# Kernel tuning notes

Hardware: AMD Instinct MI355X
Metric: run time of the kernel (lower is better)

## Reference

```python
import jax, jax.numpy as jnp
import numpy as np

N_NODES = 50000


def _glorot(key, fan_in, fan_out):
    limit = float(np.sqrt(6.0 / (fan_in + fan_out)))
    return jax.random.uniform(key, (fan_in, fan_out), jnp.float32, -limit, limit)


def setup_inputs() -> dict:
    key = jax.random.key(0)
    k_x, k_src, k_dst, k1, k2, k3 = jax.random.split(key, 6)
    x = jax.random.normal(k_x, (N_NODES, 128), dtype=jnp.float32)
    src = jax.random.randint(k_src, (800000,), 0, N_NODES)
    dst = jax.random.randint(k_dst, (800000,), 0, N_NODES)
    edge_index = jnp.stack([src, dst]).astype(jnp.int64)  # [2, E]
    W1 = _glorot(k1, 128, 96)
    W2 = _glorot(k2, 96, 96)
    W3 = _glorot(k3, 96, 40)
    b1 = jnp.zeros((96,), jnp.float32)
    b2 = jnp.zeros((96,), jnp.float32)
    b3 = jnp.zeros((40,), jnp.float32)
    return {"x": x, "W1": W1, "b1": b1, "W2": W2, "b2": b2,
            "W3": W3, "b3": b3, "edge_index": edge_index}


def _aggregate(x, src, dst):
    # sparse adj SpMM with 'add' reduce: out[dst] += x[src]
    return jax.ops.segment_sum(x[src], dst, num_segments=N_NODES)


def reference(x, W1, b1, W2, b2, W3, b3, edge_index):
    src, dst = edge_index[0], edge_index[1]
    # layer 1: aggregate -> linear -> relu (dropout identity in eval)
    h = jax.nn.relu(_aggregate(x, src, dst) @ W1 + b1)
    # layer 2
    h = jax.nn.relu(_aggregate(h, src, dst) @ W2 + b2)
    # layer 3 + log_softmax
    logits = _aggregate(h, src, dst) @ W3 + b3
    return jax.nn.log_softmax(logits, axis=-1)
```

## Files before the change

### kernel.cpp

```cpp
#include <hip/hip_runtime.h>
#include <math.h>

typedef __attribute__((ext_vector_type(8))) short bf16x8;
typedef __attribute__((ext_vector_type(4))) float f32x4;

__device__ __forceinline__ unsigned short f2bf(float f) {
  unsigned u = __float_as_uint(f);
  u += 0x7fffu + ((u >> 16) & 1u);
  return (unsigned short)(u >> 16);
}
__device__ __forceinline__ float bflo(unsigned u) { return __uint_as_float(u << 16); }
__device__ __forceinline__ float bfhi(unsigned u) { return __uint_as_float(u & 0xffff0000u); }


constexpr int CB = 64;

__global__ __launch_bounds__(256) void count_pack(const int* __restrict__ dst,
                                                  int* __restrict__ partial, int E,
                                                  const float* __restrict__ W1,
                                                  const float* __restrict__ W2,
                                                  const float* __restrict__ W3,
                                                  unsigned short* __restrict__ Wp1,
                                                  unsigned short* __restrict__ Wp2,
                                                  unsigned short* __restrict__ Wp3) {
  int tid = threadIdx.x;
  if (blockIdx.x < CB) {
    __shared__ int bkt[256];
    bkt[tid] = 0;
    __syncthreads();
    int E4 = E >> 2;
    const int4* d4 = (const int4*)dst;
    for (int i = blockIdx.x * 256 + tid; i < E4; i += CB * 256) {
      int4 d = d4[i];
      atomicAdd(&bkt[d.x >> 8], 1);
      atomicAdd(&bkt[d.y >> 8], 1);
      atomicAdd(&bkt[d.z >> 8], 1);
      atomicAdd(&bkt[d.w >> 8], 1);
    }
    if (blockIdx.x == 0 && tid < (E & 3)) atomicAdd(&bkt[dst[E4 * 4 + tid] >> 8], 1);
    __syncthreads();
    partial[blockIdx.x * 256 + tid] = bkt[tid];
    return;
  }
  int gid = (blockIdx.x - CB) * 256 + tid;
  const float* W;
  unsigned short* Wp;
  int t, NCTT, M, MV;
  if (gid < 1536) {
    W = W1; Wp = Wp1; t = gid; NCTT = 6; M = 96; MV = 96;
  } else if (gid < 2688) {
    W = W2; Wp = Wp2; t = gid - 1536; NCTT = 6; M = 96; MV = 96;
  } else if (gid < 3264) {
    W = W3; Wp = Wp3; t = gid - 2688; NCTT = 3; M = 40; MV = 40;
  } else {
    return;
  }
  int lane = t & 63;
  int frag = t >> 6;
  int s = frag / NCTT;
  int ct = frag - s * NCTT;
  int colv = ct * 16 + (lane & 15);
  int k0 = s * 32 + (lane >> 4) * 8;
  union { unsigned short s[8]; uint4 u; } pk;
#pragma unroll
  for (int j = 0; j < 8; ++j) {
    float v = (colv < MV) ? W[(k0 + j) * M + colv] : 0.f;
    pk.s[j] = f2bf(v);
  }
  ((uint4*)Wp)[t] = pk.u;
}

__global__ __launch_bounds__(256) void scan_kernel(const int* __restrict__ partial,
                                                   int* __restrict__ gstart,
                                                   int* __restrict__ gcur,
                                                   int* __restrict__ row_ptr,
                                                   int NB, int N, int E) {
  int tid = threadIdx.x;
  int s = 0;
#pragma unroll 8
  for (int i = 0; i < CB; ++i) s += partial[i * 256 + tid];
  __shared__ int sm[256];
  sm[tid] = s;
  __syncthreads();
  for (int off = 1; off < 256; off <<= 1) {
    int u = (tid >= off) ? sm[tid - off] : 0;
    __syncthreads();
    sm[tid] += u;
    __syncthreads();
  }
  int excl = sm[tid] - s;
  if (tid < NB) { gstart[tid] = excl; gcur[tid] = excl; }
  if (tid == NB - 1) gstart[NB] = sm[tid];
  if (tid == 0) row_ptr[N] = E;
}

__global__ __launch_bounds__(256) void bin_gemm1(const int* __restrict__ src,
                                                 const int* __restrict__ dst,
                                                 int* __restrict__ gcur,
                                                 int* __restrict__ packed, int E, int NB,
                                                 int NBIN, const float* __restrict__ x,
                                                 const unsigned short* __restrict__ Wp1,
                                                 unsigned short* __restrict__ Tb, int N) {
  int tid = threadIdx.x;
  if (blockIdx.x < NBIN) {
    __shared__ int lcnt[256];
    __shared__ int gbase[256];
    lcnt[tid] = 0;
    __syncthreads();
    int idx = blockIdx.x * 256 + tid;
    int E4 = E >> 2;
    int sv[4], dv[4], lv[4];
    int cnt = 0;
    if (idx < E4) {
      int4 s4 = ((const int4*)src)[idx];
      int4 d4 = ((const int4*)dst)[idx];
      sv[0] = s4.x; sv[1] = s4.y; sv[2] = s4.z; sv[3] = s4.w;
      dv[0] = d4.x; dv[1] = d4.y; dv[2] = d4.z; dv[3] = d4.w;
      cnt = 4;
    } else if (idx == E4 && (E & 3)) {
      int tl = E & 3;
      for (int i = 0; i < tl; ++i) { sv[i] = src[E4 * 4 + i]; dv[i] = dst[E4 * 4 + i]; }
      cnt = tl;
    }
    for (int i = 0; i < cnt; ++i) lv[i] = atomicAdd(&lcnt[dv[i] >> 8], 1);
    __syncthreads();
    if (tid < NB) gbase[tid] = atomicAdd(&gcur[tid], lcnt[tid]);
    __syncthreads();
    for (int i = 0; i < cnt; ++i) {
      int b = dv[i] >> 8;
      packed[gbase[b] + lv[i]] = ((dv[i] & 255) << 16) | (sv[i] & 0xffff);
    }
    return;
  }
  int bx = blockIdx.x - NBIN;
  int wid = tid >> 6;
  int lane = tid & 63;
  int rt = bx * 4 + wid;
  if (rt * 16 >= N) return;
  int quad = lane >> 4;
  int lm = lane & 15;
  union BU { uint4 u; bf16x8 v; };
  f32x4 acc[6];
#pragma unroll
  for (int c = 0; c < 6; ++c) acc[c] = (f32x4){0.f, 0.f, 0.f, 0.f};
  int row = rt * 16 + lm;
  if (row >= N) row = N - 1;
  const uint4* wp4 = (const uint4*)Wp1;
#pragma unroll
  for (int s = 0; s < 4; ++s) {
    int k0 = s * 32 + quad * 8;
    const float* Af = x + (size_t)row * 128 + k0;
    float4 x0 = *(const float4*)(Af);
    float4 x1 = *(const float4*)(Af + 4);
    union { unsigned short s[8]; bf16x8 v; } au;
    au.s[0] = f2bf(x0.x); au.s[1] = f2bf(x0.y); au.s[2] = f2bf(x0.z); au.s[3] = f2bf(x0.w);
    au.s[4] = f2bf(x1.x); au.s[5] = f2bf(x1.y); au.s[6] = f2bf(x1.z); au.s[7] = f2bf(x1.w);
#pragma unroll
    for (int c = 0; c < 6; ++c) {
      BU bu;
      bu.u = wp4[(s * 6 + c) * 64 + lane];
      acc[c] = __builtin_amdgcn_mfma_f32_16x16x32_bf16(au.v, bu.v, acc[c], 0, 0, 0);
    }
  }
#pragma unroll
  for (int c = 0; c < 6; ++c) {
    int colv = c * 16 + lm;
#pragma unroll
    for (int r = 0; r < 4; ++r) {
      int orow = rt * 16 + quad * 4 + r;
      if (orow < N) Tb[(size_t)orow * 96 + colv] = f2bf(acc[c][r]);
    }
  }
}

__global__ __launch_bounds__(256) void build_local_csr(const int* __restrict__ packed,
                                                       const int* __restrict__ gstart,
                                                       int* __restrict__ row_ptr,
                                                       int* __restrict__ col, int N) {
  __shared__ int cnt[256];
  __shared__ int sm[256];
  int b = blockIdx.x, tid = threadIdx.x;
  int gs = gstart[b], ge = gstart[b + 1];
  int me = ge - gs;
  int node0 = b << 8;
  int RL = N - node0;
  if (RL > 256) RL = 256;
  cnt[tid] = 0;
  __syncthreads();
  for (int i = tid; i < me; i += 256) atomicAdd(&cnt[packed[gs + i] >> 16], 1);
  __syncthreads();
  int v = cnt[tid];
  sm[tid] = v;
  __syncthreads();
  for (int off = 1; off < 256; off <<= 1) {
    int u = (tid >= off) ? sm[tid - off] : 0;
    __syncthreads();
    sm[tid] += u;
    __syncthreads();
  }
  int excl = gs + sm[tid] - v;
  __syncthreads();
  cnt[tid] = excl;
  if (tid < RL) row_ptr[node0 + tid] = excl;
  __syncthreads();
  for (int i = tid; i < me; i += 256) {
    int pk = packed[gs + i];
    int p = atomicAdd(&cnt[pk >> 16], 1);
    col[p] = pk & 0xffff;
  }
}


template <int NCT, int MOUT, int MVALID>
__global__ __launch_bounds__(256, 6) void fused_agg_gemm(
    const unsigned short* __restrict__ tin, const int* __restrict__ row_ptr,
    const int* __restrict__ col, const float* __restrict__ bias,
    const unsigned short* __restrict__ Wp, unsigned short* __restrict__ outp, int N) {
  constexpr int LST = 104;
  constexpr int CAP = 2048;
  __shared__ unsigned short sH[64 * LST];
  __shared__ int scol[CAP];
  __shared__ int srp[65];
  int tid = threadIdx.x;
  int node0 = blockIdx.x * 64;
  int nloc = N - node0;
  if (nloc > 64) nloc = 64;
  if (tid <= nloc) srp[tid] = row_ptr[node0 + tid];
  __syncthreads();
  int gs = srp[0];
  int me = srp[nloc] - gs;
  for (int i = tid; i < me && i < CAP; i += 256) scol[i] = col[gs + i];
  __syncthreads();

#pragma unroll
  for (int it = 0; it < 3; ++it) {
    int u = tid + it * 256;
    int nl = u / 12;
    int c = u - nl * 12;
    if (nl < nloc) {
      int beg = srp[nl] - gs;
      int end = srp[nl + 1] - gs;
      const unsigned short* tc = tin + 8 * c;
      float a0 = 0.f, a1 = 0.f, a2 = 0.f, a3 = 0.f, a4 = 0.f, a5 = 0.f, a6 = 0.f, a7 = 0.f;
      int e = beg;
      for (; e + 3 < end; e += 4) {
        int s0 = (e < CAP) ? scol[e] : col[gs + e];
        int s1 = (e + 1 < CAP) ? scol[e + 1] : col[gs + e + 1];
        int s2 = (e + 2 < CAP) ? scol[e + 2] : col[gs + e + 2];
        int s3 = (e + 3 < CAP) ? scol[e + 3] : col[gs + e + 3];
        uint4 u0 = *(const uint4*)(tc + (size_t)s0 * 96);
        uint4 u1 = *(const uint4*)(tc + (size_t)s1 * 96);
        uint4 u2 = *(const uint4*)(tc + (size_t)s2 * 96);
        uint4 u3 = *(const uint4*)(tc + (size_t)s3 * 96);
        a0 += bflo(u0.x); a1 += bfhi(u0.x); a2 += bflo(u0.y); a3 += bfhi(u0.y);
        a4 += bflo(u0.z); a5 += bfhi(u0.z); a6 += bflo(u0.w); a7 += bfhi(u0.w);
        a0 += bflo(u1.x); a1 += bfhi(u1.x); a2 += bflo(u1.y); a3 += bfhi(u1.y);
        a4 += bflo(u1.z); a5 += bfhi(u1.z); a6 += bflo(u1.w); a7 += bfhi(u1.w);
        a0 += bflo(u2.x); a1 += bfhi(u2.x); a2 += bflo(u2.y); a3 += bfhi(u2.y);
        a4 += bflo(u2.z); a5 += bfhi(u2.z); a6 += bflo(u2.w); a7 += bfhi(u2.w);
        a0 += bflo(u3.x); a1 += bfhi(u3.x); a2 += bflo(u3.y); a3 += bfhi(u3.y);
        a4 += bflo(u3.z); a5 += bfhi(u3.z); a6 += bflo(u3.w); a7 += bfhi(u3.w);
      }
      for (; e < end; ++e) {
        int s0 = (e < CAP) ? scol[e] : col[gs + e];
        uint4 u4 = *(const uint4*)(tc + (size_t)s0 * 96);
        a0 += bflo(u4.x); a1 += bfhi(u4.x); a2 += bflo(u4.y); a3 += bfhi(u4.y);
        a4 += bflo(u4.z); a5 += bfhi(u4.z); a6 += bflo(u4.w); a7 += bfhi(u4.w);
      }
      const float* b = bias + 8 * c;
      union { unsigned short s[8]; uint4 u; } pk;
      pk.s[0] = f2bf(fmaxf(a0 + b[0], 0.f));
      pk.s[1] = f2bf(fmaxf(a1 + b[1], 0.f));
      pk.s[2] = f2bf(fmaxf(a2 + b[2], 0.f));
      pk.s[3] = f2bf(fmaxf(a3 + b[3], 0.f));
      pk.s[4] = f2bf(fmaxf(a4 + b[4], 0.f));
      pk.s[5] = f2bf(fmaxf(a5 + b[5], 0.f));
      pk.s[6] = f2bf(fmaxf(a6 + b[6], 0.f));
      pk.s[7] = f2bf(fmaxf(a7 + b[7], 0.f));
      *(uint4*)&sH[nl * LST + c * 8] = pk.u;
    }
  }
  __syncthreads();

  int wid = tid >> 6;
  int lane = tid & 63;
  int rt16 = wid * 16;
  if (node0 + rt16 >= N) return;
  int quad = lane >> 4;
  int lm = lane & 15;
  union BU { uint4 u; bf16x8 v; };
  f32x4 acc[NCT];
#pragma unroll
  for (int c = 0; c < NCT; ++c) acc[c] = (f32x4){0.f, 0.f, 0.f, 0.f};
  const uint4* wp4 = (const uint4*)Wp;
#pragma unroll
  for (int s = 0; s < 3; ++s) {
    BU au;
    au.u = *(const uint4*)&sH[(rt16 + lm) * LST + s * 32 + quad * 8];
#pragma unroll
    for (int c = 0; c < NCT; ++c) {
      BU bu;
      bu.u = wp4[(s * NCT + c) * 64 + lane];
      acc[c] = __builtin_amdgcn_mfma_f32_16x16x32_bf16(au.v, bu.v, acc[c], 0, 0, 0);
    }
  }
#pragma unroll
  for (int c = 0; c < NCT; ++c) {
    int colv = c * 16 + lm;
    if (colv >= MVALID) continue;
#pragma unroll
    for (int r = 0; r < 4; ++r) {
      int orow = node0 + rt16 + quad * 4 + r;
      if (orow < N) outp[(size_t)orow * MOUT + colv] = f2bf(acc[c][r]);
    }
  }
}

__global__ __launch_bounds__(256) void agg_lsm_bf16(const unsigned short* __restrict__ t,
                                                    const int* __restrict__ row_ptr,
                                                    const int* __restrict__ col,
                                                    const float* __restrict__ bias,
                                                    float* __restrict__ out, int N) {
  constexpr int CAPL = 1024;
  __shared__ int scol[CAPL];
  __shared__ int srp[17];
  int tid = threadIdx.x;
  int node0 = blockIdx.x * 16;
  int nloc = N - node0;
  if (nloc > 16) nloc = 16;
  if (tid <= nloc) srp[tid] = row_ptr[node0 + tid];
  __syncthreads();
  int gs = srp[0];
  int me = srp[nloc] - gs;
  for (int i = tid; i < me && i < CAPL; i += 256) scol[i] = col[gs + i];
  __syncthreads();

  int nl = tid >> 4;
  int c = tid & 15;
  bool act = (c < 10) && (nl < nloc);
  int ceff = (c < 10) ? c : 0;
  const unsigned short* tc = t + 4 * ceff;
  float v0 = 0.f, v1 = 0.f, v2 = 0.f, v3 = 0.f;
  if (act) {
    int beg = srp[nl] - gs;
    int end = srp[nl + 1] - gs;
    int e = beg;
    for (; e + 3 < end; e += 4) {
      int s0 = (e < CAPL) ? scol[e] : col[gs + e];
      int s1 = (e + 1 < CAPL) ? scol[e + 1] : col[gs + e + 1];
      int s2 = (e + 2 < CAPL) ? scol[e + 2] : col[gs + e + 2];
      int s3 = (e + 3 < CAPL) ? scol[e + 3] : col[gs + e + 3];
      uint2 u = *(const uint2*)(tc + (size_t)s0 * 40);
      uint2 w = *(const uint2*)(tc + (size_t)s1 * 40);
      uint2 y = *(const uint2*)(tc + (size_t)s2 * 40);
      uint2 z = *(const uint2*)(tc + (size_t)s3 * 40);
      v0 += bflo(u.x); v1 += bfhi(u.x); v2 += bflo(u.y); v3 += bfhi(u.y);
      v0 += bflo(w.x); v1 += bfhi(w.x); v2 += bflo(w.y); v3 += bfhi(w.y);
      v0 += bflo(y.x); v1 += bfhi(y.x); v2 += bflo(y.y); v3 += bfhi(y.y);
      v0 += bflo(z.x); v1 += bfhi(z.x); v2 += bflo(z.y); v3 += bfhi(z.y);
    }
    for (; e < end; ++e) {
      int s0 = (e < CAPL) ? scol[e] : col[gs + e];
      uint2 u = *(const uint2*)(tc + (size_t)s0 * 40);
      v0 += bflo(u.x); v1 += bfhi(u.x); v2 += bflo(u.y); v3 += bfhi(u.y);
    }
  }
  const float* bb = bias + 4 * ceff;
  v0 += bb[0]; v1 += bb[1]; v2 += bb[2]; v3 += bb[3];
  float m = act ? fmaxf(fmaxf(v0, v1), fmaxf(v2, v3)) : -__builtin_inff();
#pragma unroll
  for (int off = 8; off; off >>= 1) m = fmaxf(m, __shfl_xor(m, off, 64));
  float ex = act ? (__expf(v0 - m) + __expf(v1 - m) + __expf(v2 - m) + __expf(v3 - m)) : 0.f;
#pragma unroll
  for (int off = 8; off; off >>= 1) ex += __shfl_xor(ex, off, 64);
  if (act) {
    int node = node0 + nl;
    float l = m + __logf(ex);
    float* o = out + (size_t)node * 40 + 4 * c;
    o[0] = v0 - l; o[1] = v1 - l; o[2] = v2 - l; o[3] = v3 - l;
  }
}


extern "C" void kernel_launch(void* const* d_in, const int* in_sizes, int n_in,
                              void* d_out, int out_size, void* d_ws, size_t ws_size,
                              hipStream_t stream) {
  const float* x  = (const float*)d_in[0];
  const float* W1 = (const float*)d_in[1];
  const float* b1 = (const float*)d_in[2];
  const float* W2 = (const float*)d_in[3];
  const float* b2 = (const float*)d_in[4];
  const float* W3 = (const float*)d_in[5];
  const float* b3 = (const float*)d_in[6];
  const int* edge = (const int*)d_in[7];

  int N = in_sizes[0] / 128;
  int E = in_sizes[7] / 2;
  const int* srcp = edge;
  const int* dstp = edge + E;

  char* p = (char*)d_ws;
  auto alloc = [&](size_t bytes) {
    char* r = p;
    p += (bytes + 255) & ~size_t(255);
    return r;
  };
  int NB = (N + 255) >> 8;
  int* partial = (int*)alloc((size_t)CB * 256 * 4);
  int* gstart  = (int*)alloc((size_t)(NB + 1) * 4);
  int* gcur    = (int*)alloc((size_t)NB * 4);
  int* row_ptr = (int*)alloc((size_t)(N + 1) * 4);
  int* packed  = (int*)alloc((size_t)E * 4);
  int* col     = (int*)alloc((size_t)E * 4);
  unsigned short* Wp1 = (unsigned short*)alloc(1536 * 8 * 2);
  unsigned short* Wp2 = (unsigned short*)alloc(1152 * 8 * 2);
  unsigned short* Wp3 = (unsigned short*)alloc(576 * 8 * 2);
  unsigned short* Tb  = (unsigned short*)alloc((size_t)N * 96 * 2);
  unsigned short* T2b = (unsigned short*)alloc((size_t)N * 96 * 2);
  unsigned short* T3b = (unsigned short*)alloc((size_t)N * 40 * 2);

  int E4 = E >> 2;
  int nbin = (E4 + ((E & 3) ? 1 : 0) + 255) / 256;
  int GB = ((N + 15) / 16 + 3) / 4;
  int FB = (N + 63) / 64;

  count_pack<<<CB + 13, 256, 0, stream>>>(dstp, partial, E, W1, W2, W3, Wp1, Wp2, Wp3);
  scan_kernel<<<1, 256, 0, stream>>>(partial, gstart, gcur, row_ptr, NB, N, E);
  bin_gemm1<<<nbin + GB, 256, 0, stream>>>(srcp, dstp, gcur, packed, E, NB, nbin,
                                           x, Wp1, Tb, N);
  build_local_csr<<<NB, 256, 0, stream>>>(packed, gstart, row_ptr, col, N);
  fused_agg_gemm<6, 96, 96><<<FB, 256, 0, stream>>>(Tb, row_ptr, col, b1, Wp2, T2b, N);
  fused_agg_gemm<3, 40, 40><<<FB, 256, 0, stream>>>(T2b, row_ptr, col, b2, Wp3, T3b, N);
  agg_lsm_bf16<<<(N + 15) / 16, 256, 0, stream>>>(T3b, row_ptr, col, b3, (float*)d_out, N);
}
```

Baseline: 203.1 us.

## Bin edges into 128-node buckets with block-local staged coalesced scatter

Bucket width drops from 256 to 128 nodes, giving about 391 buckets, and the count and scan kernels widen to 512 entries. Each binning block now takes 4096 edges, sorts them locally in LDS by bucket, then writes runs contiguously into the global packed array, replacing scattered per-edge writes. It also raises fused_agg_gemm occupancy to 7 blocks and shrinks the column cache to 1536 entries. The costs are an in-block scan, a binary search per output element, and a larger static LDS footprint shared with the GEMM branch of bin_gemm1, which may lower that branch's occupancy.

```diff
diff --git a/kernel.cpp b/kernel.cpp
--- a/kernel.cpp
+++ b/kernel.cpp
@@ -14,6 +14,7 @@
 
 
 constexpr int CB = 64;
+constexpr int EB = 4096;
 
 __global__ __launch_bounds__(256) void count_pack(const int* __restrict__ dst,
                                                   int* __restrict__ partial, int E,
@@ -25,21 +26,23 @@
                                                   unsigned short* __restrict__ Wp3) {
   int tid = threadIdx.x;
   if (blockIdx.x < CB) {
-    __shared__ int bkt[256];
+    __shared__ int bkt[512];
     bkt[tid] = 0;
+    bkt[tid + 256] = 0;
     __syncthreads();
     int E4 = E >> 2;
     const int4* d4 = (const int4*)dst;
     for (int i = blockIdx.x * 256 + tid; i < E4; i += CB * 256) {
       int4 d = d4[i];
-      atomicAdd(&bkt[d.x >> 8], 1);
-      atomicAdd(&bkt[d.y >> 8], 1);
-      atomicAdd(&bkt[d.z >> 8], 1);
-      atomicAdd(&bkt[d.w >> 8], 1);
-    }
-    if (blockIdx.x == 0 && tid < (E & 3)) atomicAdd(&bkt[dst[E4 * 4 + tid] >> 8], 1);
-    __syncthreads();
-    partial[blockIdx.x * 256 + tid] = bkt[tid];
+      atomicAdd(&bkt[d.x >> 7], 1);
+      atomicAdd(&bkt[d.y >> 7], 1);
+      atomicAdd(&bkt[d.z >> 7], 1);
+      atomicAdd(&bkt[d.w >> 7], 1);
+    }
+    if (blockIdx.x == 0 && tid < (E & 3)) atomicAdd(&bkt[dst[E4 * 4 + tid] >> 7], 1);
+    __syncthreads();
+    partial[blockIdx.x * 512 + tid] = bkt[tid];
+    partial[blockIdx.x * 512 + tid + 256] = bkt[tid + 256];
     return;
   }
   int gid = (blockIdx.x - CB) * 256 + tid;
@@ -75,22 +78,32 @@
                                                    int* __restrict__ gcur,
                                                    int* __restrict__ row_ptr,
                                                    int NB, int N, int E) {
+  __shared__ int sm[512];
   int tid = threadIdx.x;
-  int s = 0;
+  int s0 = 0, s1 = 0;
 #pragma unroll 8
-  for (int i = 0; i < CB; ++i) s += partial[i * 256 + tid];
-  __shared__ int sm[256];
-  sm[tid] = s;
-  __syncthreads();
-  for (int off = 1; off < 256; off <<= 1) {
-    int u = (tid >= off) ? sm[tid - off] : 0;
-    __syncthreads();
-    sm[tid] += u;
-    __syncthreads();
-  }
-  int excl = sm[tid] - s;
-  if (tid < NB) { gstart[tid] = excl; gcur[tid] = excl; }
-  if (tid == NB - 1) gstart[NB] = sm[tid];
+  for (int i = 0; i < CB; ++i) {
+    s0 += partial[i * 512 + tid];
+    s1 += partial[i * 512 + tid + 256];
+  }
+  sm[tid] = s0;
+  sm[tid + 256] = s1;
+  __syncthreads();
+  for (int off = 1; off < 512; off <<= 1) {
+    int a0 = (tid >= off) ? sm[tid - off] : 0;
+    int i1 = tid + 256;
+    int a1 = (i1 >= off) ? sm[i1 - off] : 0;
+    __syncthreads();
+    sm[tid] += a0;
+    sm[i1] += a1;
+    __syncthreads();
+  }
+  int e0 = sm[tid] - s0;
+  int e1 = sm[tid + 256] - s1;
+  if (tid < NB) { gstart[tid] = e0; gcur[tid] = e0; }
+  int b1 = tid + 256;
+  if (b1 < NB) { gstart[b1] = e1; gcur[b1] = e1; }
+  if (tid == 255) gstart[NB] = sm[511];
   if (tid == 0) row_ptr[N] = E;
 }
 
@@ -101,34 +114,83 @@
                                                  int NBIN, const float* __restrict__ x,
                                                  const unsigned short* __restrict__ Wp1,
                                                  unsigned short* __restrict__ Tb, int N) {
+  __shared__ int lcnt[512];
+  __shared__ int lstart[512];
+  __shared__ int gbase[512];
+  __shared__ int cur[512];
+  __shared__ int stage[EB];
   int tid = threadIdx.x;
   if (blockIdx.x < NBIN) {
-    __shared__ int lcnt[256];
-    __shared__ int gbase[256];
     lcnt[tid] = 0;
-    __syncthreads();
-    int idx = blockIdx.x * 256 + tid;
+    lcnt[tid + 256] = 0;
+    __syncthreads();
     int E4 = E >> 2;
-    int sv[4], dv[4], lv[4];
-    int cnt = 0;
-    if (idx < E4) {
-      int4 s4 = ((const int4*)src)[idx];
-      int4 d4 = ((const int4*)dst)[idx];
-      sv[0] = s4.x; sv[1] = s4.y; sv[2] = s4.z; sv[3] = s4.w;
-      dv[0] = d4.x; dv[1] = d4.y; dv[2] = d4.z; dv[3] = d4.w;
-      cnt = 4;
-    } else if (idx == E4 && (E & 3)) {
-      int tl = E & 3;
-      for (int i = 0; i < tl; ++i) { sv[i] = src[E4 * 4 + i]; dv[i] = dst[E4 * 4 + i]; }
-      cnt = tl;
-    }
-    for (int i = 0; i < cnt; ++i) lv[i] = atomicAdd(&lcnt[dv[i] >> 8], 1);
-    __syncthreads();
-    if (tid < NB) gbase[tid] = atomicAdd(&gcur[tid], lcnt[tid]);
-    __syncthreads();
-    for (int i = 0; i < cnt; ++i) {
-      int b = dv[i] >> 8;
-      packed[gbase[b] + lv[i]] = ((dv[i] & 255) << 16) | (sv[i] & 0xffff);
+    int base4 = blockIdx.x * (EB >> 2);
+    int sv[16], dv[16];
+    int nv = 0;
+#pragma unroll
+    for (int j = 0; j < 4; ++j) {
+      int idx4 = base4 + j * 256 + tid;
+      if (idx4 < E4 && idx4 < base4 + (EB >> 2)) {
+        int4 s4 = ((const int4*)src)[idx4];
+        int4 d4 = ((const int4*)dst)[idx4];
+        sv[j * 4 + 0] = s4.x; dv[j * 4 + 0] = d4.x;
+        sv[j * 4 + 1] = s4.y; dv[j * 4 + 1] = d4.y;
+        sv[j * 4 + 2] = s4.z; dv[j * 4 + 2] = d4.z;
+        sv[j * 4 + 3] = s4.w; dv[j * 4 + 3] = d4.w;
+        nv = j * 4 + 4;
+      }
+    }
+#pragma unroll
+    for (int i = 0; i < 16; ++i)
+      if (i < nv) atomicAdd(&lcnt[dv[i] >> 7], 1);
+    bool last = (blockIdx.x == NBIN - 1);
+    int tl = E & 3;
+    if (last && tid == 0)
+      for (int t = 0; t < tl; ++t) atomicAdd(&lcnt[dst[E4 * 4 + t] >> 7], 1);
+    __syncthreads();
+    lstart[tid] = lcnt[tid];
+    lstart[tid + 256] = lcnt[tid + 256];
+    __syncthreads();
+    for (int off = 1; off < 512; off <<= 1) {
+      int a0 = (tid >= off) ? lstart[tid - off] : 0;
+      int i1 = tid + 256;
+      int a1 = (i1 >= off) ? lstart[i1 - off] : 0;
+      __syncthreads();
+      lstart[tid] += a0;
+      lstart[i1] += a1;
+      __syncthreads();
+    }
+    int e0 = lstart[tid] - lcnt[tid];
+    int e1 = lstart[tid + 256] - lcnt[tid + 256];
+    __syncthreads();
+    lstart[tid] = e0; cur[tid] = e0;
+    lstart[tid + 256] = e1; cur[tid + 256] = e1;
+    __syncthreads();
+#pragma unroll
+    for (int i = 0; i < 16; ++i)
+      if (i < nv) {
+        int b = dv[i] >> 7;
+        int p = atomicAdd(&cur[b], 1);
+        stage[p] = ((dv[i] & 127) << 16) | (sv[i] & 0xffff);
+      }
+    if (last && tid == 0)
+      for (int t = 0; t < tl; ++t) {
+        int d = dst[E4 * 4 + t], s = src[E4 * 4 + t];
+        int p = atomicAdd(&cur[d >> 7], 1);
+        stage[p] = ((d & 127) << 16) | (s & 0xffff);
+      }
+    if (lcnt[tid]) gbase[tid] = atomicAdd(&gcur[tid], lcnt[tid]);
+    if (lcnt[tid + 256]) gbase[tid + 256] = atomicAdd(&gcur[tid + 256], lcnt[tid + 256]);
+    __syncthreads();
+    int meB = lstart[511] + lcnt[511];
+    for (int i = tid; i < meB; i += 256) {
+      int lo = 0, hi = 511;
+      while (lo < hi) {
+        int mid = (lo + hi + 1) >> 1;
+        if (lstart[mid] <= i) lo = mid; else hi = mid - 1;
+      }
+      packed[gbase[lo] + (i - lstart[lo])] = stage[i];
     }
     return;
   }
@@ -177,31 +239,31 @@
                                                        const int* __restrict__ gstart,
                                                        int* __restrict__ row_ptr,
                                                        int* __restrict__ col, int N) {
-  __shared__ int cnt[256];
-  __shared__ int sm[256];
+  __shared__ int cnt[128];
+  __shared__ int sm[128];
   int b = blockIdx.x, tid = threadIdx.x;
   int gs = gstart[b], ge = gstart[b + 1];
   int me = ge - gs;
-  int node0 = b << 8;
+  int node0 = b << 7;
   int RL = N - node0;
-  if (RL > 256) RL = 256;
-  cnt[tid] = 0;
+  if (RL > 128) RL = 128;
+  if (tid < 128) cnt[tid] = 0;
   __syncthreads();
   for (int i = tid; i < me; i += 256) atomicAdd(&cnt[packed[gs + i] >> 16], 1);
   __syncthreads();
-  int v = cnt[tid];
-  sm[tid] = v;
-  __syncthreads();
-  for (int off = 1; off < 256; off <<= 1) {
-    int u = (tid >= off) ? sm[tid - off] : 0;
-    __syncthreads();
-    sm[tid] += u;
-    __syncthreads();
-  }
-  int excl = gs + sm[tid] - v;
-  __syncthreads();
-  cnt[tid] = excl;
-  if (tid < RL) row_ptr[node0 + tid] = excl;
+  if (tid < 128) sm[tid] = cnt[tid];
+  __syncthreads();
+  for (int off = 1; off < 128; off <<= 1) {
+    int u = (tid >= off && tid < 128) ? sm[tid - off] : 0;
+    __syncthreads();
+    if (tid < 128) sm[tid] += u;
+    __syncthreads();
+  }
+  if (tid < 128) {
+    int excl = gs + sm[tid] - cnt[tid];
+    cnt[tid] = excl;
+    if (tid < RL) row_ptr[node0 + tid] = excl;
+  }
   __syncthreads();
   for (int i = tid; i < me; i += 256) {
     int pk = packed[gs + i];
@@ -212,12 +274,12 @@
 
 
 template <int NCT, int MOUT, int MVALID>
-__global__ __launch_bounds__(256, 6) void fused_agg_gemm(
+__global__ __launch_bounds__(256, 7) void fused_agg_gemm(
     const unsigned short* __restrict__ tin, const int* __restrict__ row_ptr,
     const int* __restrict__ col, const float* __restrict__ bias,
     const unsigned short* __restrict__ Wp, unsigned short* __restrict__ outp, int N) {
   constexpr int LST = 104;
-  constexpr int CAP = 2048;
+  constexpr int CAP = 1536;
   __shared__ unsigned short sH[64 * LST];
   __shared__ int scol[CAP];
   __shared__ int srp[65];
@@ -405,8 +467,8 @@
     p += (bytes + 255) & ~size_t(255);
     return r;
   };
-  int NB = (N + 255) >> 8;
-  int* partial = (int*)alloc((size_t)CB * 256 * 4);
+  int NB = (N + 127) >> 7;
+  int* partial = (int*)alloc((size_t)CB * 512 * 4);
   int* gstart  = (int*)alloc((size_t)(NB + 1) * 4);
   int* gcur    = (int*)alloc((size_t)NB * 4);
   int* row_ptr = (int*)alloc((size_t)(N + 1) * 4);
@@ -419,14 +481,13 @@
   unsigned short* T2b = (unsigned short*)alloc((size_t)N * 96 * 2);
   unsigned short* T3b = (unsigned short*)alloc((size_t)N * 40 * 2);
 
-  int E4 = E >> 2;
-  int nbin = (E4 + ((E & 3) ? 1 : 0) + 255) / 256;
+  int NBIN = (E + EB - 1) / EB;
   int GB = ((N + 15) / 16 + 3) / 4;
   int FB = (N + 63) / 64;
 
   count_pack<<<CB + 13, 256, 0, stream>>>(dstp, partial, E, W1, W2, W3, Wp1, Wp2, Wp3);
   scan_kernel<<<1, 256, 0, stream>>>(partial, gstart, gcur, row_ptr, NB, N, E);
-  bin_gemm1<<<nbin + GB, 256, 0, stream>>>(srcp, dstp, gcur, packed, E, NB, nbin,
+  bin_gemm1<<<NBIN + GB, 256, 0, stream>>>(srcp, dstp, gcur, packed, E, NB, NBIN,
                                            x, Wp1, Tb, N);
   build_local_csr<<<NB, 256, 0, stream>>>(packed, gstart, row_ptr, col, N);
   fused_agg_gemm<6, 96, 96><<<FB, 256, 0, stream>>>(Tb, row_ptr, col, b1, Wp2, T2b, N);
```

New measurement: 196.6 us. 3.2% less time.
